# Optimization experiments

Measured on AMD Instinct MI355X. Metric: run time of the kernel, lower is better.

Reference implementation:

```python
import jax, jax.numpy as jnp
import numpy as np
import math

B, S, H = 2, 2048, 1024
NH, HD = 16, 64
MAX_SCALE = 4


def setup_inputs() -> dict:
    key = jax.random.key(0)
    ks = jax.random.split(key, 8)
    s = 0.02
    return {
        "x": jax.random.normal(ks[0], (B, S, H), dtype=jnp.float32),
        "Wqkv": jax.random.normal(ks[1], (H, 3 * H), dtype=jnp.float32) * s,
        "bqkv": jnp.zeros((3 * H,), dtype=jnp.float32),
        "Wout": jax.random.normal(ks[2], (H, H), dtype=jnp.float32) * s,
        "bout": jnp.zeros((H,), dtype=jnp.float32),
        "Wscale": jax.random.normal(ks[3], (H, MAX_SCALE), dtype=jnp.float32) * s,
        "bscale": jnp.zeros((MAX_SCALE,), dtype=jnp.float32),
    }


def reference(x, Wqkv, bqkv, Wout, bout, Wscale, bscale):
    b, s, h = x.shape
    inv_sqrt_hd = 1.0 / math.sqrt(HD)
    # qkv projection -> [3, b, nh, s, hd]
    qkv = (x @ Wqkv + bqkv).reshape(b, s, 3, NH, HD).transpose(2, 0, 3, 1, 4)
    q, k, v = qkv[0], qkv[1], qkv[2]
    # per-token soft weights over scales [b, s, max_scale]
    scale_weights = jax.nn.softmax(x @ Wscale + bscale, axis=-1)
    out = jnp.zeros((b, NH, s, HD), dtype=x.dtype)
    for scale_idx in range(MAX_SCALE):
        dilation = 2 ** scale_idx
        kd = k[:, :, ::dilation]  # strided (dilated) gather of keys
        vd = v[:, :, ::dilation]
        scores = jnp.einsum("bhqd,bhkd->bhqk", q, kd) * inv_sqrt_hd
        attn = jax.nn.softmax(scores, axis=-1)
        o = jnp.einsum("bhqk,bhkd->bhqd", attn, vd)
        w = scale_weights[:, :, scale_idx][:, None, :, None]  # [b,1,s,1]
        out = out + o * w
    out = out.transpose(0, 2, 1, 3).reshape(b, s, h)
    return out @ Wout + bout
```

## Files before the change

### kernel.cpp

```cpp
#include <hip/hip_runtime.h>
#include <stdint.h>

typedef unsigned short u16;
typedef __attribute__((ext_vector_type(8))) __bf16 bf8v;
typedef __attribute__((ext_vector_type(4))) float f4v;
typedef __attribute__((ext_vector_type(16))) float f16v;
typedef __attribute__((ext_vector_type(4))) uint32_t u32x4;

#define BB 2
#define SS 2048
#define HH 1024

#define OFF_Q   0u
#define OFF_K0  8388608u
#define OFF_V0  24117248u
#define OFF_V1  32505856u
#define OFF_V2  36700160u
#define OFF_V3  38797312u
#define OFF_WQT 39845888u
#define OFF_WOT 46137344u
#define OFF_XB  48234496u
#define OFF_SCW 56623104u

__device__ __forceinline__ u16 f2bf(float f) {
    union { float f; uint32_t u; } v; v.f = f;
    uint32_t r = v.u + 0x7fffu + ((v.u >> 16) & 1u);
    return (u16)(r >> 16);
}
__device__ __forceinline__ uint32_t pk2(float a, float b) {
    return (uint32_t)f2bf(a) | ((uint32_t)f2bf(b) << 16);
}
__device__ __forceinline__ uint32_t pkt2(float a, float b) {
    union { float f; uint32_t u; } x, y; x.f = a; y.f = b;
    return (x.u >> 16) | (y.u & 0xffff0000u);
}

__device__ __forceinline__ void gl2lds16(const u16* g, u16* l) {
    __builtin_amdgcn_global_load_lds(
        (__attribute__((address_space(1))) void*)g,
        (__attribute__((address_space(3))) void*)l, 16, 0, 0);
}

__global__ __launch_bounds__(256) void xscale_kernel(const float* __restrict__ x,
                                                     const float* __restrict__ Wscale,
                                                     const float* __restrict__ bscale,
                                                     u16* __restrict__ xb,
                                                     float* __restrict__ scw) {
    const int row  = blockIdx.x;
    const int t    = threadIdx.x;
    const int lane = t & 63;
    const int wid  = t >> 6;
    __shared__ float part[4][4];

    float4 v = *(const float4*)&x[(size_t)row * 1024 + t * 4];
    uint2 pk; pk.x = pk2(v.x, v.y); pk.y = pk2(v.z, v.w);
    *(uint2*)&xb[(size_t)row * 1024 + t * 4] = pk;

    float4 w0 = *(const float4*)&Wscale[(t * 4 + 0) * 4];
    float4 w1 = *(const float4*)&Wscale[(t * 4 + 1) * 4];
    float4 w2 = *(const float4*)&Wscale[(t * 4 + 2) * 4];
    float4 w3 = *(const float4*)&Wscale[(t * 4 + 3) * 4];
    float a0 = v.x * w0.x + v.y * w1.x + v.z * w2.x + v.w * w3.x;
    float a1 = v.x * w0.y + v.y * w1.y + v.z * w2.y + v.w * w3.y;
    float a2 = v.x * w0.z + v.y * w1.z + v.z * w2.z + v.w * w3.z;
    float a3 = v.x * w0.w + v.y * w1.w + v.z * w2.w + v.w * w3.w;
    for (int off = 1; off < 64; off <<= 1) {
        a0 += __shfl_xor(a0, off); a1 += __shfl_xor(a1, off);
        a2 += __shfl_xor(a2, off); a3 += __shfl_xor(a3, off);
    }
    if (lane == 0) {
        part[wid][0] = a0; part[wid][1] = a1;
        part[wid][2] = a2; part[wid][3] = a3;
    }
    __syncthreads();
    if (t == 0) {
        a0 = part[0][0] + part[1][0] + part[2][0] + part[3][0] + bscale[0];
        a1 = part[0][1] + part[1][1] + part[2][1] + part[3][1] + bscale[1];
        a2 = part[0][2] + part[1][2] + part[2][2] + part[3][2] + bscale[2];
        a3 = part[0][3] + part[1][3] + part[2][3] + part[3][3] + bscale[3];
        float mx = fmaxf(fmaxf(a0, a1), fmaxf(a2, a3));
        float e0 = __expf(a0 - mx), e1 = __expf(a1 - mx);
        float e2 = __expf(a2 - mx), e3 = __expf(a3 - mx);
        float inv = 1.f / (e0 + e1 + e2 + e3);
        float4 o = {e0 * inv, e1 * inv, e2 * inv, e3 * inv};
        *(float4*)&scw[(size_t)row * 4] = o;
    }
}

__global__ __launch_bounds__(256) void wconv_kernel(const float* __restrict__ W,
                                                    u16* __restrict__ Wt,
                                                    int N, int K) {
    __shared__ float tile[64][69];
    const int tid = threadIdx.x;
    const int n0 = blockIdx.x * 64, k0 = blockIdx.y * 64;
    const int r = tid >> 4, c4 = (tid & 15) * 4;
#pragma unroll
    for (int it = 0; it < 4; it++) {
        float4 v = *(const float4*)&W[(size_t)(k0 + it * 16 + r) * N + n0 + c4];
        tile[it * 16 + r][c4 + 0] = v.x; tile[it * 16 + r][c4 + 1] = v.y;
        tile[it * 16 + r][c4 + 2] = v.z; tile[it * 16 + r][c4 + 3] = v.w;
    }
    __syncthreads();
#pragma unroll
    for (int it = 0; it < 4; it++) {
        int n = it * 16 + r;
        uint2 pk;
        pk.x = pk2(tile[c4 + 0][n], tile[c4 + 1][n]);
        pk.y = pk2(tile[c4 + 2][n], tile[c4 + 3][n]);
        *(uint2*)&Wt[(size_t)(n0 + n) * K + k0 + c4] = pk;
    }
}

template<int MODE>
__global__ __launch_bounds__(256) void gemm_bt(const u16* __restrict__ A,
                                               const u16* __restrict__ Bt,
                                               const float* __restrict__ bias,
                                               void* __restrict__ Cp,
                                               int N, int K) {
    __shared__ __align__(16) u16 At[2][128 * 32];
    __shared__ __align__(16) u16 Btl[2][128 * 32];
    const int tid  = threadIdx.x;
    const int lane = tid & 63;
    const int wid  = tid >> 6;
    const int l15  = lane & 15;
    const int quad = lane >> 4;
    const int wm = wid & 1, wn = wid >> 1;
    const int m0 = blockIdx.y * 128;
    const int n0 = blockIdx.x * 128;
    const int cA0 = wid * 2, cA1 = wid * 2 + 1;
    const int lrow = lane >> 2;
    const int lcol = (lane & 3) * 8;

    f4v acc[4][4];
#pragma unroll
    for (int i = 0; i < 4; i++)
#pragma unroll
        for (int j = 0; j < 4; j++) acc[i][j] = (f4v){0.f, 0.f, 0.f, 0.f};

    gl2lds16(A  + (size_t)(m0 + cA0 * 16 + lrow) * K + lcol, At[0]  + cA0 * 512);
    gl2lds16(A  + (size_t)(m0 + cA1 * 16 + lrow) * K + lcol, At[0]  + cA1 * 512);
    gl2lds16(Bt + (size_t)(n0 + cA0 * 16 + lrow) * K + lcol, Btl[0] + cA0 * 512);
    gl2lds16(Bt + (size_t)(n0 + cA1 * 16 + lrow) * K + lcol, Btl[0] + cA1 * 512);
    __syncthreads();

    int cur = 0;
    for (int kc = 0; kc < K; kc += 32) {
        if (kc + 32 < K) {
            gl2lds16(A  + (size_t)(m0 + cA0 * 16 + lrow) * K + kc + 32 + lcol, At[cur ^ 1]  + cA0 * 512);
            gl2lds16(A  + (size_t)(m0 + cA1 * 16 + lrow) * K + kc + 32 + lcol, At[cur ^ 1]  + cA1 * 512);
            gl2lds16(Bt + (size_t)(n0 + cA0 * 16 + lrow) * K + kc + 32 + lcol, Btl[cur ^ 1] + cA0 * 512);
            gl2lds16(Bt + (size_t)(n0 + cA1 * 16 + lrow) * K + kc + 32 + lcol, Btl[cur ^ 1] + cA1 * 512);
        }
        bf8v af[4], bf[4];
#pragma unroll
        for (int t = 0; t < 4; t++) {
            af[t] = *(const bf8v*)&At[cur][(wm * 64 + t * 16 + l15) * 32 + quad * 8];
            bf[t] = *(const bf8v*)&Btl[cur][(wn * 64 + t * 16 + l15) * 32 + quad * 8];
        }
#pragma unroll
        for (int ti = 0; ti < 4; ti++)
#pragma unroll
            for (int tj = 0; tj < 4; tj++)
                acc[ti][tj] = __builtin_amdgcn_mfma_f32_16x16x32_bf16(af[ti], bf[tj], acc[ti][tj], 0, 0, 0);
        __syncthreads();
        cur ^= 1;
    }

    if (MODE == 0) {
#pragma unroll
        for (int ti = 0; ti < 4; ti++)
#pragma unroll
            for (int tj = 0; tj < 4; tj++)
#pragma unroll
                for (int r = 0; r < 4; r++) {
                    int m = m0 + wm * 64 + ti * 16 + quad * 4 + r;
                    int n = n0 + wn * 64 + tj * 16 + l15;
                    ((float*)Cp)[(size_t)m * N + n] = acc[ti][tj][r] + bias[n];
                }
    } else {
        char* ws = (char*)Cp;
        u16* Qd = (u16*)ws;
        u16* K0 = (u16*)(ws + OFF_K0);
        u16* V0 = (u16*)(ws + OFF_V0); u16* V1 = (u16*)(ws + OFF_V1);
        u16* V2 = (u16*)(ws + OFF_V2); u16* V3 = (u16*)(ws + OFF_V3);
        const int region = n0 >> 10;
        if (region == 0) {
#pragma unroll
            for (int ti = 0; ti < 4; ti++)
#pragma unroll
                for (int tj = 0; tj < 4; tj++)
#pragma unroll
                    for (int r = 0; r < 4; r++) {
                        int m = m0 + wm * 64 + ti * 16 + quad * 4 + r;
                        int n = n0 + wn * 64 + tj * 16 + l15;
                        Qd[(size_t)m * 1024 + n] = f2bf(acc[ti][tj][r] + bias[n]);
                    }
        } else if (region == 1) {
#pragma unroll
            for (int ti = 0; ti < 4; ti++)
#pragma unroll
                for (int tj = 0; tj < 4; tj++) {
                    int n  = n0 + wn * 64 + tj * 16 + l15;
                    int nk = n - 1024;
                    int h = nk >> 6, hd = nk & 63;
#pragma unroll
                    for (int r = 0; r < 4; r++) {
                        int m = m0 + wm * 64 + ti * 16 + quad * 4 + r;
                        int bb = m >> 11, tok = m & 2047;
                        int bh = bb * 16 + h;
                        u16 bv = f2bf((acc[ti][tj][r] + bias[n]) * 0.18033688f);
                        K0[((size_t)bh * 2048 + tok) * 64 + hd] = bv;
                    }
                }
        } else {
#pragma unroll
            for (int ti = 0; ti < 4; ti++)
#pragma unroll
                for (int tj = 0; tj < 4; tj++) {
                    int n  = n0 + wn * 64 + tj * 16 + l15;
                    int nv = n - 2048;
                    int h = nv >> 6, hd = nv & 63;
                    int tokb = m0 + wm * 64 + ti * 16 + quad * 4;
                    int bb = tokb >> 11, tok = tokb & 2047;
                    int bh = bb * 16 + h;
                    float v0 = acc[ti][tj][0] + bias[n];
                    float v1 = acc[ti][tj][1] + bias[n];
                    float v2 = acc[ti][tj][2] + bias[n];
                    float v3 = acc[ti][tj][3] + bias[n];
                    u16 c0 = f2bf(v0), c1 = f2bf(v1), c2 = f2bf(v2), c3 = f2bf(v3);
                    uint2 pk;
                    pk.x = (uint32_t)c0 | ((uint32_t)c1 << 16);
                    pk.y = (uint32_t)c2 | ((uint32_t)c3 << 16);
                    int tokp = (tok & ~15) | ((tok & 4) << 1) | ((tok & 8) >> 1);
                    *(uint2*)&V0[((size_t)bh * 64 + hd) * 2048 + tokp] = pk;
                    int kk = tok >> 1;
                    int v1p = (kk & ~15) | ((kk & 2) << 2) | ((kk & 12) >> 1);
                    *(uint32_t*)&V1[((size_t)bh * 64 + hd) * 1024 + v1p] =
                        (uint32_t)c0 | ((uint32_t)c2 << 16);
                    int t2 = tok >> 2;
                    int v2i = (t2 & ~15) | ((t2 & 1) << 3) | ((t2 & 15) >> 1);
                    V2[((size_t)bh * 64 + hd) * 512 + v2i] = c0;
                    if (!(quad & 1)) V3[((size_t)bh * 64 + hd) * 256 + (tok >> 3)] = c0;
                }
        }
    }
}

__global__ __launch_bounds__(256, 2) void attn_kernel(const char* __restrict__ ws) {
    __shared__ __align__(16) u16 smem[15872];
    u16* Kt0  = smem;
    u16* Kt1  = smem + 2304;
    u16* Vt0  = smem + 4608;
    u16* Vt1  = smem + 7168;
    u16* V1t0 = smem + 9728;
    u16* V1t1 = smem + 11264;
    u16* V2t  = smem + 12800;
    u16* V3t  = smem + 14336;

    const u16* Qd    = (const u16*)(ws + OFF_Q);
    const float* scw = (const float*)(ws + OFF_SCW);
    u16* attnb       = (u16*)(ws + OFF_Q);

    const int tid  = threadIdx.x;
    const int lane = tid & 63;
    const int wid  = tid >> 6;
    const int l31  = lane & 31;
    const int half = lane >> 5;

    const int f   = blockIdx.x + 16 * blockIdx.y + 256 * blockIdx.z;
    const int xcd = f & 7, fj = f >> 3;
    const int grp = xcd * 4 + (fj >> 4);
    const int qt  = fj & 15;
    const int b = grp >> 4, h = grp & 15;
    const int q  = qt * 128 + wid * 32 + l31;
    const int bh = b * 16 + h;

    const int skey = tid >> 3;
    const int shd8 = (tid & 7) * 8;
    const int svhd = tid >> 2;
    const int svk8 = (tid & 3) * 8;
    const int vi4  = (tid & 3) * 4;

    bf8v qf[4];
#pragma unroll
    for (int ks = 0; ks < 4; ks++)
        qf[ks] = *(const bf8v*)(Qd + (size_t)(b * SS + q) * 1024 + h * 64 + ks * 16 + half * 8);

    const u16* Kb  = (const u16*)(ws + OFF_K0) + (size_t)bh * (2048 * 64);
    const u16* Vb0 = (const u16*)(ws + OFF_V0) + (size_t)bh * (64 * 2048);
    const u16* Vb1 = (const u16*)(ws + OFF_V1) + (size_t)bh * (64 * 1024);
    const u16* Vb2 = (const u16*)(ws + OFF_V2) + (size_t)bh * (64 * 512);
    const u16* Vb3 = (const u16*)(ws + OFF_V3) + (size_t)bh * (64 * 256);

    f16v oacc0[2], oacc1[2], oacc2[2], oacc3[2];
#pragma unroll
    for (int ht = 0; ht < 2; ht++)
#pragma unroll
        for (int r = 0; r < 16; r++) {
            oacc0[ht][r] = 0.f; oacc1[ht][r] = 0.f;
            oacc2[ht][r] = 0.f; oacc3[ht][r] = 0.f;
        }
    float ls0 = 0.f, ls1 = 0.f, ls2 = 0.f, ls3 = 0.f;

    uint4 kr  = *(const uint4*)(Kb + (size_t)skey * 64 + shd8);
    uint4 vr  = *(const uint4*)(Vb0 + (size_t)svhd * 2048 + svk8);
    uint2 v1r = *(const uint2*)(Vb1 + (size_t)svhd * 1024 + vi4);
    uint2 v2r = *(const uint2*)(Vb2 + (size_t)svhd * 512 + vi4);
    uint2 v3r = *(const uint2*)(Vb3 + (size_t)svhd * 256 + vi4);
    *(uint4*)&Kt0[skey * 72 + shd8] = kr;
    *(uint4*)&Vt0[svhd * 40 + svk8] = vr;
    *(uint2*)&V1t0[svhd * 24 + vi4] = v1r;
    kr  = *(const uint4*)(Kb + (size_t)(32 + skey) * 64 + shd8);
    vr  = *(const uint4*)(Vb0 + (size_t)svhd * 2048 + 32 + svk8);
    v1r = *(const uint2*)(Vb1 + (size_t)svhd * 1024 + 16 + vi4);
    __syncthreads();

    uint32_t Pa[4], Pb[4];
    union uu { u32x4 u; bf8v b; };

    for (int cc = 0; cc < 64; cc += 4) {
#pragma unroll
        for (int ph = 0; ph < 4; ph++) {
            const int c = cc + ph;
            u16* Ktc  = (ph & 1) ? Kt1 : Kt0;
            u16* Vtc  = (ph & 1) ? Vt1 : Vt0;
            u16* V1tc = (ph & 1) ? V1t1 : V1t0;
            u16* Ktn  = (ph & 1) ? Kt0 : Kt1;
            u16* Vtn  = (ph & 1) ? Vt0 : Vt1;
            u16* V1tn = (ph & 1) ? V1t0 : V1t1;

            f16v sa;
#pragma unroll
            for (int r = 0; r < 16; r++) sa[r] = 0.f;
#pragma unroll
            for (int ks = 0; ks < 4; ks++) {
                bf8v ka = *(const bf8v*)&Ktc[l31 * 72 + ks * 16 + half * 8];
                sa = __builtin_amdgcn_mfma_f32_32x32x16_bf16(ka, qf[ks], sa, 0, 0, 0);
            }
            float e[16];
#pragma unroll
            for (int g = 0; g < 4; g++) {
                float e0 = exp2f(sa[g * 4 + 0]);
                float e1 = exp2f(sa[g * 4 + 1]);
                float e2 = exp2f(sa[g * 4 + 2]);
                float e3 = exp2f(sa[g * 4 + 3]);
                e[g * 4 + 0] = e0; e[g * 4 + 1] = e1;
                e[g * 4 + 2] = e2; e[g * 4 + 3] = e3;
                ls0 += (e0 + e1) + (e2 + e3);
                ls1 += e0 + e2;
                ls2 += e0;
                if (!half) ls3 += e0;
            }
            uint32_t F00 = pkt2(e[0],  e[1]),  F01 = pkt2(e[2],  e[3]);
            uint32_t F02 = pkt2(e[4],  e[5]),  F03 = pkt2(e[6],  e[7]);
            uint32_t F10 = pkt2(e[8],  e[9]),  F11 = pkt2(e[10], e[11]);
            uint32_t F12 = pkt2(e[12], e[13]), F13 = pkt2(e[14], e[15]);
            uint32_t G0 = pkt2(e[0],  e[2]),   G1 = pkt2(e[4],  e[6]);
            uint32_t G2 = pkt2(e[8],  e[10]),  G3 = pkt2(e[12], e[14]);
            Pa[ph] = pkt2(e[0], e[4]);
            Pb[ph] = pkt2(e[8], e[12]);

            if (c + 1 < 64) {
                *(uint4*)&Ktn[skey * 72 + shd8] = kr;
                *(uint4*)&Vtn[svhd * 40 + svk8] = vr;
                *(uint2*)&V1tn[svhd * 24 + vi4] = v1r;
            }
            if (!(ph & 1)) {
                *(uint2*)&V2t[svhd * 24 + vi4] = v2r;
                if (ph == 0)
                    *(uint2*)&V3t[svhd * 24 + vi4] = v3r;
            }
            if (c + 2 < 64) {
                kr  = *(const uint4*)(Kb + (size_t)((c + 2) * 32 + skey) * 64 + shd8);
                vr  = *(const uint4*)(Vb0 + (size_t)svhd * 2048 + (c + 2) * 32 + svk8);
                v1r = *(const uint2*)(Vb1 + (size_t)svhd * 1024 + (c + 2) * 16 + vi4);
                if (!((c + 2) & 1))
                    v2r = *(const uint2*)(Vb2 + (size_t)svhd * 512 + (c + 2) * 8 + vi4);
                if (!((c + 2) & 3))
                    v3r = *(const uint2*)(Vb3 + (size_t)svhd * 256 + (c + 2) * 4 + vi4);
            }
            {
                uu p0; p0.u = (u32x4){F00, F01, F02, F03};
#pragma unroll
                for (int ht = 0; ht < 2; ht++) {
                    bf8v va = *(const bf8v*)&Vtc[(ht * 32 + l31) * 40 + half * 8];
                    oacc0[ht] = __builtin_amdgcn_mfma_f32_32x32x16_bf16(va, p0.b, oacc0[ht], 0, 0, 0);
                }
                uu p1; p1.u = (u32x4){F10, F11, F12, F13};
#pragma unroll
                for (int ht = 0; ht < 2; ht++) {
                    bf8v va = *(const bf8v*)&Vtc[(ht * 32 + l31) * 40 + 16 + half * 8];
                    oacc0[ht] = __builtin_amdgcn_mfma_f32_32x32x16_bf16(va, p1.b, oacc0[ht], 0, 0, 0);
                }
            }
            {
                uu ps; ps.u = (u32x4){G0, G1, G2, G3};
#pragma unroll
                for (int ht = 0; ht < 2; ht++) {
                    bf8v va1 = *(const bf8v*)&V1tc[(ht * 32 + l31) * 24 + half * 8];
                    oacc1[ht] = __builtin_amdgcn_mfma_f32_32x32x16_bf16(va1, ps.b, oacc1[ht], 0, 0, 0);
                }
            }
            if (ph == 1 || ph == 3) {
                uu p2; p2.u = (u32x4){Pa[ph - 1], Pb[ph - 1], Pa[ph], Pb[ph]};
#pragma unroll
                for (int ht = 0; ht < 2; ht++) {
                    bf8v va2 = *(const bf8v*)&V2t[(ht * 32 + l31) * 24 + half * 8];
                    oacc2[ht] = __builtin_amdgcn_mfma_f32_32x32x16_bf16(va2, p2.b, oacc2[ht], 0, 0, 0);
                }
            }
            if (ph == 3) {
                uint32_t t0 = __shfl_xor(Pa[2], 32);
                uint32_t t1 = __shfl_xor(Pb[2], 32);
                uint32_t t2 = __shfl_xor(Pa[3], 32);
                uint32_t t3 = __shfl_xor(Pb[3], 32);
                uint32_t w0 = half ? t0 : Pa[0];
                uint32_t w1 = half ? t1 : Pb[0];
                uint32_t w2 = half ? t2 : Pa[1];
                uint32_t w3 = half ? t3 : Pb[1];
                uu p3; p3.u = (u32x4){w0, w1, w2, w3};
#pragma unroll
                for (int ht = 0; ht < 2; ht++) {
                    bf8v va3 = *(const bf8v*)&V3t[(ht * 32 + l31) * 24 + half * 8];
                    oacc3[ht] = __builtin_amdgcn_mfma_f32_32x32x16_bf16(va3, p3.b, oacc3[ht], 0, 0, 0);
                }
            }
            __syncthreads();
        }
    }
    ls0 += __shfl_xor(ls0, 32);
    ls1 += __shfl_xor(ls1, 32);
    ls2 += __shfl_xor(ls2, 32);
    ls3 += __shfl_xor(ls3, 32);
    float4 sw = *(const float4*)&scw[(size_t)(b * SS + q) * 4];
    float w0 = sw.x / ls0, w1 = sw.y / ls1, w2 = sw.z / ls2, w3 = sw.w / ls3;

    const size_t base = (size_t)(b * SS + q) * 1024 + h * 64;
#pragma unroll
    for (int ht = 0; ht < 2; ht++)
#pragma unroll
        for (int g = 0; g < 4; g++) {
            float f0 = w0 * oacc0[ht][g * 4 + 0] + w1 * oacc1[ht][g * 4 + 0]
                     + w2 * oacc2[ht][g * 4 + 0] + w3 * oacc3[ht][g * 4 + 0];
            float f1 = w0 * oacc0[ht][g * 4 + 1] + w1 * oacc1[ht][g * 4 + 1]
                     + w2 * oacc2[ht][g * 4 + 1] + w3 * oacc3[ht][g * 4 + 1];
            float f2 = w0 * oacc0[ht][g * 4 + 2] + w1 * oacc1[ht][g * 4 + 2]
                     + w2 * oacc2[ht][g * 4 + 2] + w3 * oacc3[ht][g * 4 + 2];
            float f3 = w0 * oacc0[ht][g * 4 + 3] + w1 * oacc1[ht][g * 4 + 3]
                     + w2 * oacc2[ht][g * 4 + 3] + w3 * oacc3[ht][g * 4 + 3];
            uint2 pk;
            pk.x = pk2(f0, f1);
            pk.y = pk2(f2, f3);
            *(uint2*)&attnb[base + ht * 32 + g * 8 + half * 4] = pk;
        }
}

extern "C" void kernel_launch(void* const* d_in, const int* in_sizes, int n_in,
                              void* d_out, int out_size, void* d_ws, size_t ws_size,
                              hipStream_t stream) {
    const float* x      = (const float*)d_in[0];
    const float* Wqkv   = (const float*)d_in[1];
    const float* bqkv   = (const float*)d_in[2];
    const float* Wout   = (const float*)d_in[3];
    const float* bout   = (const float*)d_in[4];
    const float* Wscale = (const float*)d_in[5];
    const float* bscale = (const float*)d_in[6];
    float* out = (float*)d_out;

    char* ws = (char*)d_ws;
    u16*   wqt   = (u16*)(ws + OFF_WQT);
    u16*   wot   = (u16*)(ws + OFF_WOT);
    u16*   xb    = (u16*)(ws + OFF_XB);
    u16*   attnb = (u16*)(ws + OFF_Q);
    float* scw   = (float*)(ws + OFF_SCW);

    xscale_kernel<<<dim3(4096), dim3(256), 0, stream>>>(x, Wscale, bscale, xb, scw);
    wconv_kernel<<<dim3(48, 16), dim3(256), 0, stream>>>(Wqkv, wqt, 3072, 1024);
    wconv_kernel<<<dim3(16, 16), dim3(256), 0, stream>>>(Wout, wot, 1024, 1024);
    gemm_bt<1><<<dim3(24, 32), dim3(256), 0, stream>>>(xb, wqt, bqkv, (void*)ws, 3072, 1024);
    attn_kernel<<<dim3(16, 16, 2), dim3(256), 0, stream>>>(ws);
    gemm_bt<0><<<dim3(8, 32), dim3(256), 0, stream>>>(attnb, wot, bout, (void*)out, 1024, 1024);
}
```

Before: 264.1 us.

## Replace GEMM direct-to-LDS loads with register prefetch and hoist attention tile stores

The GEMM drops double-buffered global_load_lds staging. It now prefetches the next K-chunk into registers and stores it into a single padded LDS tile (row stride 40) between two barriers, which avoids bank conflicts on the fragment reads and halves LDS use. In the attention loop, the LDS stores of the next K/V tiles and the global prefetch of the tile after that move ahead of the QK MFMA, so memory latency overlaps more compute. The cost is an extra barrier per K-step in the GEMM and more live registers.

Result: no change. 260.6 us (-1.3%).

```diff
diff --git a/kernel.cpp b/kernel.cpp
--- a/kernel.cpp
+++ b/kernel.cpp
@@ -33,12 +33,6 @@
 __device__ __forceinline__ uint32_t pkt2(float a, float b) {
     union { float f; uint32_t u; } x, y; x.f = a; y.f = b;
     return (x.u >> 16) | (y.u & 0xffff0000u);
-}
-
-__device__ __forceinline__ void gl2lds16(const u16* g, u16* l) {
-    __builtin_amdgcn_global_load_lds(
-        (__attribute__((address_space(1))) void*)g,
-        (__attribute__((address_space(3))) void*)l, 16, 0, 0);
 }
 
 __global__ __launch_bounds__(256) void xscale_kernel(const float* __restrict__ x,
@@ -117,8 +111,8 @@
                                                const float* __restrict__ bias,
                                                void* __restrict__ Cp,
                                                int N, int K) {
-    __shared__ __align__(16) u16 At[2][128 * 32];
-    __shared__ __align__(16) u16 Btl[2][128 * 32];
+    __shared__ __align__(16) u16 At[128 * 40];
+    __shared__ __align__(16) u16 Btl[128 * 40];
     const int tid  = threadIdx.x;
     const int lane = tid & 63;
     const int wid  = tid >> 6;
@@ -127,9 +121,8 @@
     const int wm = wid & 1, wn = wid >> 1;
     const int m0 = blockIdx.y * 128;
     const int n0 = blockIdx.x * 128;
-    const int cA0 = wid * 2, cA1 = wid * 2 + 1;
-    const int lrow = lane >> 2;
-    const int lcol = (lane & 3) * 8;
+    const int srow = tid >> 2;
+    const int sc8  = (tid & 3) * 8;
 
     f4v acc[4][4];
 #pragma unroll
@@ -137,33 +130,35 @@
 #pragma unroll
         for (int j = 0; j < 4; j++) acc[i][j] = (f4v){0.f, 0.f, 0.f, 0.f};
 
-    gl2lds16(A  + (size_t)(m0 + cA0 * 16 + lrow) * K + lcol, At[0]  + cA0 * 512);
-    gl2lds16(A  + (size_t)(m0 + cA1 * 16 + lrow) * K + lcol, At[0]  + cA1 * 512);
-    gl2lds16(Bt + (size_t)(n0 + cA0 * 16 + lrow) * K + lcol, Btl[0] + cA0 * 512);
-    gl2lds16(Bt + (size_t)(n0 + cA1 * 16 + lrow) * K + lcol, Btl[0] + cA1 * 512);
-    __syncthreads();
-
-    int cur = 0;
+    uint4 pa0 = *(const uint4*)(A  + (size_t)(m0 + srow) * K + sc8);
+    uint4 pa1 = *(const uint4*)(A  + (size_t)(m0 + srow + 64) * K + sc8);
+    uint4 pb0 = *(const uint4*)(Bt + (size_t)(n0 + srow) * K + sc8);
+    uint4 pb1 = *(const uint4*)(Bt + (size_t)(n0 + srow + 64) * K + sc8);
+
     for (int kc = 0; kc < K; kc += 32) {
+        __syncthreads();
+        *(uint4*)&At[srow * 40 + sc8]         = pa0;
+        *(uint4*)&At[(srow + 64) * 40 + sc8]  = pa1;
+        *(uint4*)&Btl[srow * 40 + sc8]        = pb0;
+        *(uint4*)&Btl[(srow + 64) * 40 + sc8] = pb1;
+        __syncthreads();
         if (kc + 32 < K) {
-            gl2lds16(A  + (size_t)(m0 + cA0 * 16 + lrow) * K + kc + 32 + lcol, At[cur ^ 1]  + cA0 * 512);
-            gl2lds16(A  + (size_t)(m0 + cA1 * 16 + lrow) * K + kc + 32 + lcol, At[cur ^ 1]  + cA1 * 512);
-            gl2lds16(Bt + (size_t)(n0 + cA0 * 16 + lrow) * K + kc + 32 + lcol, Btl[cur ^ 1] + cA0 * 512);
-            gl2lds16(Bt + (size_t)(n0 + cA1 * 16 + lrow) * K + kc + 32 + lcol, Btl[cur ^ 1] + cA1 * 512);
+            pa0 = *(const uint4*)(A  + (size_t)(m0 + srow) * K + kc + 32 + sc8);
+            pa1 = *(const uint4*)(A  + (size_t)(m0 + srow + 64) * K + kc + 32 + sc8);
+            pb0 = *(const uint4*)(Bt + (size_t)(n0 + srow) * K + kc + 32 + sc8);
+            pb1 = *(const uint4*)(Bt + (size_t)(n0 + srow + 64) * K + kc + 32 + sc8);
         }
         bf8v af[4], bf[4];
 #pragma unroll
         for (int t = 0; t < 4; t++) {
-            af[t] = *(const bf8v*)&At[cur][(wm * 64 + t * 16 + l15) * 32 + quad * 8];
-            bf[t] = *(const bf8v*)&Btl[cur][(wn * 64 + t * 16 + l15) * 32 + quad * 8];
+            af[t] = *(const bf8v*)&At[(wm * 64 + t * 16 + l15) * 40 + quad * 8];
+            bf[t] = *(const bf8v*)&Btl[(wn * 64 + t * 16 + l15) * 40 + quad * 8];
         }
 #pragma unroll
         for (int ti = 0; ti < 4; ti++)
 #pragma unroll
             for (int tj = 0; tj < 4; tj++)
                 acc[ti][tj] = __builtin_amdgcn_mfma_f32_16x16x32_bf16(af[ti], bf[tj], acc[ti][tj], 0, 0, 0);
-        __syncthreads();
-        cur ^= 1;
     }
 
     if (MODE == 0) {
@@ -329,6 +324,25 @@
             u16* Vtn  = (ph & 1) ? Vt0 : Vt1;
             u16* V1tn = (ph & 1) ? V1t0 : V1t1;
 
+            if (c + 1 < 64) {
+                *(uint4*)&Ktn[skey * 72 + shd8] = kr;
+                *(uint4*)&Vtn[svhd * 40 + svk8] = vr;
+                *(uint2*)&V1tn[svhd * 24 + vi4] = v1r;
+            }
+            if (!(ph & 1)) {
+                *(uint2*)&V2t[svhd * 24 + vi4] = v2r;
+                if (ph == 0)
+                    *(uint2*)&V3t[svhd * 24 + vi4] = v3r;
+            }
+            if (c + 2 < 64) {
+                kr  = *(const uint4*)(Kb + (size_t)((c + 2) * 32 + skey) * 64 + shd8);
+                vr  = *(const uint4*)(Vb0 + (size_t)svhd * 2048 + (c + 2) * 32 + svk8);
+                v1r = *(const uint2*)(Vb1 + (size_t)svhd * 1024 + (c + 2) * 16 + vi4);
+                if (!((c + 2) & 1))
+                    v2r = *(const uint2*)(Vb2 + (size_t)svhd * 512 + (c + 2) * 8 + vi4);
+                if (!((c + 2) & 3))
+                    v3r = *(const uint2*)(Vb3 + (size_t)svhd * 256 + (c + 2) * 4 + vi4);
+            }
             f16v sa;
 #pragma unroll
             for (int r = 0; r < 16; r++) sa[r] = 0.f;
@@ -360,25 +374,6 @@
             Pa[ph] = pkt2(e[0], e[4]);
             Pb[ph] = pkt2(e[8], e[12]);
 
-            if (c + 1 < 64) {
-                *(uint4*)&Ktn[skey * 72 + shd8] = kr;
-                *(uint4*)&Vtn[svhd * 40 + svk8] = vr;
-                *(uint2*)&V1tn[svhd * 24 + vi4] = v1r;
-            }
-            if (!(ph & 1)) {
-                *(uint2*)&V2t[svhd * 24 + vi4] = v2r;
-                if (ph == 0)
-                    *(uint2*)&V3t[svhd * 24 + vi4] = v3r;
-            }
-            if (c + 2 < 64) {
-                kr  = *(const uint4*)(Kb + (size_t)((c + 2) * 32 + skey) * 64 + shd8);
-                vr  = *(const uint4*)(Vb0 + (size_t)svhd * 2048 + (c + 2) * 32 + svk8);
-                v1r = *(const uint2*)(Vb1 + (size_t)svhd * 1024 + (c + 2) * 16 + vi4);
-                if (!((c + 2) & 1))
-                    v2r = *(const uint2*)(Vb2 + (size_t)svhd * 512 + (c + 2) * 8 + vi4);
-                if (!((c + 2) & 3))
-                    v3r = *(const uint2*)(Vb3 + (size_t)svhd * 256 + (c + 2) * 4 + vi4);
-            }
             {
                 uu p0; p0.u = (u32x4){F00, F01, F02, F03};
 #pragma unroll
```
